# Kernel tuning notes

Hardware: AMD Instinct MI355X
Metric: run time of the kernel (lower is better)

## Reference

```python
import jax, jax.numpy as jnp
import numpy as np

H = 1024   # hidden_size
NH = 16    # num heads
HD = H // NH


def setup_inputs() -> dict:
    key = jax.random.key(0)
    ks = jax.random.split(key, 6)
    B, S = 4, 2048
    hidden_states = jax.random.normal(ks[0], (B, S, H), dtype=jnp.float32)
    attention_mask = jnp.zeros((B, S), dtype=jnp.float32)  # additive mask
    scale = 1.0 / np.sqrt(H)
    Wq = jax.random.normal(ks[1], (H, H), dtype=jnp.float32) * scale
    Wk = jax.random.normal(ks[2], (H, H), dtype=jnp.float32) * scale
    Wv = jax.random.normal(ks[3], (H, H), dtype=jnp.float32) * scale
    Wo = jax.random.normal(ks[4], (H, H), dtype=jnp.float32) * scale
    return {"hidden_states": hidden_states, "attention_mask": attention_mask,
            "Wq": Wq, "Wk": Wk, "Wv": Wv, "Wo": Wo}


def reference(hidden_states, attention_mask, Wq, Wk, Wv, Wo):
    B, S, _ = hidden_states.shape
    scaling = HD ** -0.5
    # nn.Linear: y = x @ W.T ; split heads -> [B, NH, S, HD]
    def heads(x, W):
        return (x @ W.T).reshape(B, S, NH, HD).transpose(0, 2, 1, 3)
    q = heads(hidden_states, Wq)
    k = heads(hidden_states, Wk)
    v = heads(hidden_states, Wv)
    scores = jnp.einsum('bhqd,bhkd->bhqk', q, k) * scaling
    scores = scores + attention_mask[:, None, None, :]
    weights = jax.nn.softmax(scores, axis=-1)
    attn = jnp.einsum('bhqk,bhkd->bhqd', weights, v)
    attn = attn.transpose(0, 2, 1, 3).reshape(B, S, H)
    return attn @ Wo.T
```

## Files before the change

kernel.cpp:

```cpp
#include <hip/hip_runtime.h>
#include <hip/hip_bf16.h>

#define B_ 4
#define S_ 2048
#define H_ 1024
#define NH_ 16
#define HD_ 64
#define QSCALE 0.1803368801111204f

typedef __bf16 bf16_t;
typedef bf16_t bf16x8 __attribute__((ext_vector_type(8)));
typedef bf16_t bf16x4 __attribute__((ext_vector_type(4)));
typedef bf16_t bf16x2t __attribute__((ext_vector_type(2)));
typedef float f32x4 __attribute__((ext_vector_type(4)));
typedef unsigned u32x2 __attribute__((ext_vector_type(2)));
typedef unsigned u32x4 __attribute__((ext_vector_type(4)));

__device__ __forceinline__ f32x4 mfma16(bf16x8 a, bf16x8 b, f32x4 c) {
  return __builtin_amdgcn_mfma_f32_16x16x32_bf16(a, b, c, 0, 0, 0);
}

__device__ __forceinline__ float fast_exp2(float x) {
#if __has_builtin(__builtin_amdgcn_exp2f)
  return __builtin_amdgcn_exp2f(x);
#else
  float r;
  asm volatile("v_exp_f32 %0, %1" : "=v"(r) : "v"(x));
  return r;
#endif
}

__device__ __forceinline__ void gll16(const bf16_t* g, bf16_t* l) {
  __builtin_amdgcn_global_load_lds(
      (const __attribute__((address_space(1))) void*)g,
      (__attribute__((address_space(3))) void*)l, 16, 0, 0);
}

__device__ __forceinline__ bf16x8 frag64(const bf16_t* lds, int row,
                                         int kchunk) {
  return *(const bf16x8*)((const char*)lds + row * 128 +
                          ((kchunk ^ (row & 7)) << 4));
}

__device__ __forceinline__ void stage128(const bf16_t* gbase, int gstride,
                                         bf16_t* lds, int w, int lane) {
#pragma unroll
  for (int j = 0; j < 4; ++j) {
    int seg = w * 4 + j;
    int row = seg * 8 + (lane >> 3);
    int chunk = (lane & 7) ^ (row & 7);
    gll16(gbase + (size_t)row * gstride + chunk * 8, lds + seg * 512);
  }
}

__global__ __launch_bounds__(256) void cvt_all(
    const float* __restrict__ X, const float* __restrict__ Wq,
    const float* __restrict__ Wk, const float* __restrict__ Wv,
    const float* __restrict__ Wo, const float* __restrict__ mask,
    bf16_t* __restrict__ Xb, bf16_t* __restrict__ Wqb,
    bf16_t* __restrict__ Wkb, bf16_t* __restrict__ Wvb,
    bf16_t* __restrict__ Wob, float* __restrict__ maskl) {
  size_t i = ((size_t)blockIdx.x * 256 + threadIdx.x) * 4;
  const float* src;
  bf16_t* dst;
  size_t off;
  float scale = 1.0f;
  if (i < 8388608) {
    src = X; dst = Xb; off = i;
  } else {
    size_t j = i - 8388608;
    if (j >= 4194304) {
      size_t mo = j - 4194304;
      float4 mv = *(const float4*)(mask + mo);
      const float LOG2E = 1.4426950408889634f;
      float4 ml = {mv.x * LOG2E, mv.y * LOG2E, mv.z * LOG2E, mv.w * LOG2E};
      *(float4*)(maskl + mo) = ml;
      return;
    }
    int w = (int)(j >> 20);
    off = j & 1048575;
    switch (w) {
      case 0: src = Wq; dst = Wqb; scale = QSCALE; break;
      case 1: src = Wk; dst = Wkb; break;
      case 2: src = Wv; dst = Wvb; break;
      default: src = Wo; dst = Wob; break;
    }
  }
  float4 v = *(const float4*)(src + off);
  bf16x4 o = {(bf16_t)(v.x * scale), (bf16_t)(v.y * scale),
              (bf16_t)(v.z * scale), (bf16_t)(v.w * scale)};
  *(bf16x4*)(dst + off) = o;
}

__device__ __forceinline__ void gemm_core(const bf16_t* __restrict__ A,
                                          const bf16_t* __restrict__ Bw,
                                          int Mb, int Nb, bf16_t* As,
                                          bf16_t* Bs, f32x4 (*acc)[4], int w,
                                          int lane, int quad, int l15, int wm,
                                          int wn) {
  for (int kb = 0; kb < 16; ++kb) {
    stage128(A + (size_t)Mb * 1024 + kb * 64, 1024, As, w, lane);
    stage128(Bw + (size_t)Nb * 1024 + kb * 64, 1024, Bs, w, lane);
    __syncthreads();
#pragma unroll
    for (int kt = 0; kt < 2; ++kt) {
      bf16x8 af[4], bfr[4];
#pragma unroll
      for (int i = 0; i < 4; ++i) {
        af[i] = frag64(As, wm * 64 + i * 16 + l15, kt * 4 + quad);
        bfr[i] = frag64(Bs, wn * 64 + i * 16 + l15, kt * 4 + quad);
      }
      __builtin_amdgcn_s_setprio(1);
#pragma unroll
      for (int mt = 0; mt < 4; ++mt)
#pragma unroll
        for (int nt = 0; nt < 4; ++nt)
          acc[mt][nt] = mfma16(af[mt], bfr[nt], acc[mt][nt]);
      __builtin_amdgcn_s_setprio(0);
    }
    __syncthreads();
  }
}

__global__ __launch_bounds__(256) void gemm_qkv(
    const bf16_t* __restrict__ Xb, const bf16_t* __restrict__ Wqb,
    const bf16_t* __restrict__ Wkb, const bf16_t* __restrict__ Wvb,
    bf16_t* __restrict__ q_ws, bf16_t* __restrict__ k_ws,
    bf16_t* __restrict__ vt_ws) {
  __shared__ __align__(16) bf16_t As[8192];
  __shared__ __align__(16) bf16_t Bs[8192];
  int w = threadIdx.x >> 6, lane = threadIdx.x & 63;
  int quad = lane >> 4, l15 = lane & 15;
  int wm = w >> 1, wn = w & 1;
  int z = blockIdx.z;
  const bf16_t* A = (z == 2) ? Wvb : Xb;
  const bf16_t* Bw = (z == 0) ? Wqb : ((z == 1) ? Wkb : Xb);
  int Mb = (z == 2) ? blockIdx.y * 128 : blockIdx.x * 128;
  int Nb = (z == 2) ? blockIdx.x * 128 : blockIdx.y * 128;
  f32x4 acc[4][4] = {};
  gemm_core(A, Bw, Mb, Nb, As, Bs, acc, w, lane, quad, l15, wm, wn);
  if (z != 2) {
    bf16_t* O = (z == 0) ? q_ws : k_ws;
#pragma unroll
    for (int mt = 0; mt < 4; ++mt) {
      int m0t = Mb + wm * 64 + mt * 16;
#pragma unroll
      for (int nt = 0; nt < 4; ++nt) {
        int n0t = Nb + wn * 64 + nt * 16;
        int h = n0t >> 6, d = (n0t & 63) + l15;
#pragma unroll
        for (int r = 0; r < 4; ++r) {
          int tok = m0t + quad * 4 + r;
          int b = tok >> 11, s = tok & 2047;
          O[(((size_t)b * NH_ + h) * S_ + s) * HD_ + d] = (bf16_t)acc[mt][nt][r];
        }
      }
    }
  } else {
#pragma unroll
    for (int mt = 0; mt < 4; ++mt) {
      int m0t = Mb + wm * 64 + mt * 16;
#pragma unroll
      for (int nt = 0; nt < 4; ++nt) {
        int n0t = Nb + wn * 64 + nt * 16;
#pragma unroll
        for (int r = 0; r < 4; ++r) {
          int dg = m0t + quad * 4 + r;
          int hh = dg >> 6, d = dg & 63;
          int tok = n0t + l15;
          int b = tok >> 11, s = tok & 2047;
          vt_ws[((size_t)(b * NH_ + hh) * HD_ + d) * S_ + s] =
              (bf16_t)acc[mt][nt][r];
        }
      }
    }
  }
}

__global__ __launch_bounds__(256) void gemm_out(
    const bf16_t* __restrict__ A, const bf16_t* __restrict__ Bw,
    float* __restrict__ out) {
  __shared__ __align__(16) bf16_t As[8192];
  __shared__ __align__(16) bf16_t Bs[8192];
  int w = threadIdx.x >> 6, lane = threadIdx.x & 63;
  int quad = lane >> 4, l15 = lane & 15;
  int wm = w >> 1, wn = w & 1;
  int Mb = blockIdx.x * 128, Nb = blockIdx.y * 128;
  f32x4 acc[4][4] = {};
  gemm_core(A, Bw, Mb, Nb, As, Bs, acc, w, lane, quad, l15, wm, wn);
#pragma unroll
  for (int mt = 0; mt < 4; ++mt) {
    int m0t = Mb + wm * 64 + mt * 16;
#pragma unroll
    for (int nt = 0; nt < 4; ++nt) {
      int n0t = Nb + wn * 64 + nt * 16;
#pragma unroll
      for (int r = 0; r < 4; ++r)
        out[(size_t)(m0t + quad * 4 + r) * 1024 + n0t + l15] = acc[mt][nt][r];
    }
  }
}

__global__ __launch_bounds__(256, 3) void attn_fused(
    const bf16_t* __restrict__ Q, const bf16_t* __restrict__ K,
    const bf16_t* __restrict__ Vt, const float* __restrict__ maskl,
    bf16_t* __restrict__ Oa) {
  __shared__ __align__(16) bf16_t Ks[2][4096];
  __shared__ __align__(16) bf16_t Vs[2][4096];
  int w = threadIdx.x >> 6, lane = threadIdx.x & 63;
  int quad = lane >> 4, l15 = lane & 15;
  int bh = blockIdx.y;
  int b = bh >> 4, h = bh & 15;
  int q0 = blockIdx.x * 128 + w * 32;
  const bf16_t* Qh = Q + (size_t)bh * (S_ * HD_);
  const bf16_t* Kh = K + (size_t)bh * (S_ * HD_);
  const bf16_t* Vh = Vt + (size_t)bh * (HD_ * S_);
  const float* mb = maskl + b * S_;
  const bf16_t one_b = (bf16_t)1.0f;
  bf16x8 ones = {one_b, one_b, one_b, one_b, one_b, one_b, one_b, one_b};

  int srow[2], schunk[2], soff[2];
#pragma unroll
  for (int j = 0; j < 2; ++j) {
    int seg = w * 2 + j;
    srow[j] = seg * 8 + (lane >> 3);
    schunk[j] = (lane & 7) ^ (srow[j] & 7);
    soff[j] = seg * 512 + lane * 8;
  }

  bf16x8 qf[2][2];
#pragma unroll
  for (int nt = 0; nt < 2; ++nt)
#pragma unroll
    for (int kt = 0; kt < 2; ++kt)
      qf[nt][kt] = *(const bf16x8*)(Qh + (size_t)(q0 + nt * 16 + l15) * HD_ +
                                    kt * 32 + quad * 8);

  f32x4 oc[4][2] = {};
  f32x4 lc[2] = {};

  bf16x8 kreg[2], vreg[2];
#pragma unroll
  for (int j = 0; j < 2; ++j) {
    kreg[j] = *(const bf16x8*)(Kh + (size_t)srow[j] * HD_ + schunk[j] * 8);
    vreg[j] = *(const bf16x8*)(Vh + (size_t)srow[j] * S_ + schunk[j] * 8);
  }
#pragma unroll
  for (int j = 0; j < 2; ++j) {
    *(bf16x8*)(&Ks[0][0] + soff[j]) = kreg[j];
    *(bf16x8*)(&Vs[0][0] + soff[j]) = vreg[j];
  }
#pragma unroll
  for (int j = 0; j < 2; ++j) {
    kreg[j] = *(const bf16x8*)(Kh + (size_t)(64 * HD_) +
                               (size_t)srow[j] * HD_ + schunk[j] * 8);
    vreg[j] = *(const bf16x8*)(Vh + 64 + (size_t)srow[j] * S_ + schunk[j] * 8);
  }
  f32x4 mreg[4];
#pragma unroll
  for (int mt = 0; mt < 4; ++mt)
    mreg[mt] = *(const f32x4*)(mb + mt * 16 + quad * 4);
  __syncthreads();

  for (int c = 0; c < 32; ++c) {
    int cur = c & 1;
    if (c + 1 < 32) {
#pragma unroll
      for (int j = 0; j < 2; ++j) {
        *(bf16x8*)(&Ks[cur ^ 1][0] + soff[j]) = kreg[j];
        *(bf16x8*)(&Vs[cur ^ 1][0] + soff[j]) = vreg[j];
      }
    }
    if (c + 2 < 32) {
      const bf16_t* Kc = Kh + (size_t)(c + 2) * 64 * HD_;
      const bf16_t* Vc = Vh + (size_t)(c + 2) * 64;
#pragma unroll
      for (int j = 0; j < 2; ++j) {
        kreg[j] = *(const bf16x8*)(Kc + (size_t)srow[j] * HD_ + schunk[j] * 8);
        vreg[j] = *(const bf16x8*)(Vc + (size_t)srow[j] * S_ + schunk[j] * 8);
      }
    }
    f32x4 mcur[4];
#pragma unroll
    for (int mt = 0; mt < 4; ++mt) mcur[mt] = mreg[mt];
    if (c + 1 < 32) {
#pragma unroll
      for (int mt = 0; mt < 4; ++mt)
        mreg[mt] = *(const f32x4*)(mb + (c + 1) * 64 + mt * 16 + quad * 4);
    }
    f32x4 sc[4][2] = {};
#pragma unroll
    for (int kt = 0; kt < 2; ++kt) {
      bf16x8 kf[4];
#pragma unroll
      for (int mt = 0; mt < 4; ++mt)
        kf[mt] = frag64(Ks[cur], mt * 16 + l15, kt * 4 + quad);
      __builtin_amdgcn_s_setprio(1);
#pragma unroll
      for (int mt = 0; mt < 4; ++mt)
#pragma unroll
        for (int nt = 0; nt < 2; ++nt)
          sc[mt][nt] = mfma16(kf[mt], qf[nt][kt], sc[mt][nt]);
      __builtin_amdgcn_s_setprio(0);
    }
#pragma unroll
    for (int kt = 0; kt < 2; ++kt) {
      unsigned pk[2][2][2];
#pragma unroll
      for (int mi = 0; mi < 2; ++mi) {
        int mt = kt * 2 + mi;
#pragma unroll
        for (int nt = 0; nt < 2; ++nt) {
          f32x4 e = sc[mt][nt] + mcur[mt];
          f32x4 p;
#pragma unroll
          for (int r = 0; r < 4; ++r) p[r] = fast_exp2(e[r]);
          bf16x2t h0 = {(bf16_t)p[0], (bf16_t)p[1]};
          bf16x2t h1 = {(bf16_t)p[2], (bf16_t)p[3]};
          pk[mi][nt][0] = __builtin_bit_cast(unsigned, h0);
          pk[mi][nt][1] = __builtin_bit_cast(unsigned, h1);
        }
      }
      bf16x8 pf[2];
#pragma unroll
      for (int nt = 0; nt < 2; ++nt) {
        u32x2 a0 = __builtin_amdgcn_permlane32_swap(pk[0][nt][0],
                                                    pk[1][nt][0],
                                                    false, false);
        u32x2 b0 = __builtin_amdgcn_permlane16_swap(a0.x, a0.y, false, false);
        u32x2 a1 = __builtin_amdgcn_permlane32_swap(pk[0][nt][1],
                                                    pk[1][nt][1],
                                                    false, false);
        u32x2 b1 = __builtin_amdgcn_permlane16_swap(a1.x, a1.y, false, false);
        u32x4 pu = {b0.x, b1.x, b0.y, b1.y};
        pf[nt] = __builtin_bit_cast(bf16x8, pu);
      }
      __builtin_amdgcn_s_setprio(1);
      lc[0] = mfma16(ones, pf[0], lc[0]);
      lc[1] = mfma16(ones, pf[1], lc[1]);
#pragma unroll
      for (int dt = 0; dt < 4; ++dt) {
        bf16x8 vf = frag64(Vs[cur], dt * 16 + l15, kt * 4 + quad);
#pragma unroll
        for (int nt = 0; nt < 2; ++nt)
          oc[dt][nt] = mfma16(vf, pf[nt], oc[dt][nt]);
      }
      __builtin_amdgcn_s_setprio(0);
    }
    __syncthreads();
  }
  float inv[2] = {1.0f / lc[0][0], 1.0f / lc[1][0]};
#pragma unroll
  for (int dt = 0; dt < 4; ++dt)
#pragma unroll
    for (int nt = 0; nt < 2; ++nt) {
      bf16x4 o4;
#pragma unroll
      for (int r = 0; r < 4; ++r) o4[r] = (bf16_t)(oc[dt][nt][r] * inv[nt]);
      size_t tok = (size_t)b * S_ + q0 + nt * 16 + l15;
      *(bf16x4*)(Oa + tok * H_ + h * HD_ + dt * 16 + quad * 4) = o4;
    }
}

extern "C" void kernel_launch(void* const* d_in, const int* in_sizes, int n_in,
                              void* d_out, int out_size, void* d_ws,
                              size_t ws_size, hipStream_t stream) {
  const float* hs   = (const float*)d_in[0];
  const float* mask = (const float*)d_in[1];
  const float* Wq   = (const float*)d_in[2];
  const float* Wk   = (const float*)d_in[3];
  const float* Wv   = (const float*)d_in[4];
  const float* Wo   = (const float*)d_in[5];
  float* out = (float*)d_out;

  char* p = (char*)d_ws;
  bf16_t* Xb  = (bf16_t*)p; p += (size_t)8192 * 1024 * 2;
  bf16_t* Wqb = (bf16_t*)p; p += (size_t)1024 * 1024 * 2;
  bf16_t* Wkb = (bf16_t*)p; p += (size_t)1024 * 1024 * 2;
  bf16_t* Wvb = (bf16_t*)p; p += (size_t)1024 * 1024 * 2;
  bf16_t* Wob = (bf16_t*)p; p += (size_t)1024 * 1024 * 2;
  bf16_t* q_ws  = (bf16_t*)p; p += (size_t)8192 * 1024 * 2;
  bf16_t* k_ws  = (bf16_t*)p; p += (size_t)8192 * 1024 * 2;
  bf16_t* vt_ws = (bf16_t*)p; p += (size_t)8192 * 1024 * 2;
  float* maskl = (float*)p; p += (size_t)B_ * S_ * 4;
  bf16_t* attn_b = Xb;

  cvt_all<<<12296, 256, 0, stream>>>(hs, Wq, Wk, Wv, Wo, mask, Xb, Wqb, Wkb,
                                     Wvb, Wob, maskl);
  gemm_qkv<<<dim3(64, 8, 3), 256, 0, stream>>>(Xb, Wqb, Wkb, Wvb, q_ws, k_ws,
                                               vt_ws);
  attn_fused<<<dim3(16, 64), 256, 0, stream>>>(q_ws, k_ws, vt_ws, maskl,
                                               attn_b);
  gemm_out<<<dim3(64, 8), 256, 0, stream>>>(attn_b, Wob, out);
}
```

Baseline: 304.0 us.

## Stage K/V tiles via direct global-to-LDS loads and drop setprio hints

Replaces the register-staged double buffering of K and V tiles (global load into VGPRs, then an LDS store one iteration later) with direct global_load_lds transfers straight into the alternate LDS buffer, prefetching one chunk ahead instead of two. The aim is to free VGPRs and remove the LDS write instructions and their latency from the main loop. It also removes the s_setprio wrappers around the MFMA blocks and switches exp2 to the OCML native exp2. The prefetch distance shrinks and correctness now depends on the async LDS loads being complete before the barrier.

```diff
diff --git a/kernel.cpp b/kernel.cpp
--- a/kernel.cpp
+++ b/kernel.cpp
@@ -20,14 +20,9 @@
   return __builtin_amdgcn_mfma_f32_16x16x32_bf16(a, b, c, 0, 0, 0);
 }
 
+extern "C" __device__ float __ocml_native_exp2_f32(float);
 __device__ __forceinline__ float fast_exp2(float x) {
-#if __has_builtin(__builtin_amdgcn_exp2f)
-  return __builtin_amdgcn_exp2f(x);
-#else
-  float r;
-  asm volatile("v_exp_f32 %0, %1" : "=v"(r) : "v"(x));
-  return r;
-#endif
+  return __ocml_native_exp2_f32(x);
 }
 
 __device__ __forceinline__ void gll16(const bf16_t* g, bf16_t* l) {
@@ -219,13 +214,13 @@
   const bf16_t one_b = (bf16_t)1.0f;
   bf16x8 ones = {one_b, one_b, one_b, one_b, one_b, one_b, one_b, one_b};
 
-  int srow[2], schunk[2], soff[2];
+  int srow[2], schunk[2], lseg[2];
 #pragma unroll
   for (int j = 0; j < 2; ++j) {
     int seg = w * 2 + j;
     srow[j] = seg * 8 + (lane >> 3);
     schunk[j] = (lane & 7) ^ (srow[j] & 7);
-    soff[j] = seg * 512 + lane * 8;
+    lseg[j] = seg * 512;
   }
 
   bf16x8 qf[2][2];
@@ -239,22 +234,10 @@
   f32x4 oc[4][2] = {};
   f32x4 lc[2] = {};
 
-  bf16x8 kreg[2], vreg[2];
 #pragma unroll
   for (int j = 0; j < 2; ++j) {
-    kreg[j] = *(const bf16x8*)(Kh + (size_t)srow[j] * HD_ + schunk[j] * 8);
-    vreg[j] = *(const bf16x8*)(Vh + (size_t)srow[j] * S_ + schunk[j] * 8);
-  }
-#pragma unroll
-  for (int j = 0; j < 2; ++j) {
-    *(bf16x8*)(&Ks[0][0] + soff[j]) = kreg[j];
-    *(bf16x8*)(&Vs[0][0] + soff[j]) = vreg[j];
-  }
-#pragma unroll
-  for (int j = 0; j < 2; ++j) {
-    kreg[j] = *(const bf16x8*)(Kh + (size_t)(64 * HD_) +
-                               (size_t)srow[j] * HD_ + schunk[j] * 8);
-    vreg[j] = *(const bf16x8*)(Vh + 64 + (size_t)srow[j] * S_ + schunk[j] * 8);
+    gll16(Kh + (size_t)srow[j] * HD_ + schunk[j] * 8, &Ks[0][0] + lseg[j]);
+    gll16(Vh + (size_t)srow[j] * S_ + schunk[j] * 8, &Vs[0][0] + lseg[j]);
   }
   f32x4 mreg[4];
 #pragma unroll
@@ -265,19 +248,14 @@
   for (int c = 0; c < 32; ++c) {
     int cur = c & 1;
     if (c + 1 < 32) {
+      const bf16_t* Kc = Kh + (size_t)(c + 1) * 64 * HD_;
+      const bf16_t* Vc = Vh + (size_t)(c + 1) * 64;
 #pragma unroll
       for (int j = 0; j < 2; ++j) {
-        *(bf16x8*)(&Ks[cur ^ 1][0] + soff[j]) = kreg[j];
-        *(bf16x8*)(&Vs[cur ^ 1][0] + soff[j]) = vreg[j];
-      }
-    }
-    if (c + 2 < 32) {
-      const bf16_t* Kc = Kh + (size_t)(c + 2) * 64 * HD_;
-      const bf16_t* Vc = Vh + (size_t)(c + 2) * 64;
-#pragma unroll
-      for (int j = 0; j < 2; ++j) {
-        kreg[j] = *(const bf16x8*)(Kc + (size_t)srow[j] * HD_ + schunk[j] * 8);
-        vreg[j] = *(const bf16x8*)(Vc + (size_t)srow[j] * S_ + schunk[j] * 8);
+        gll16(Kc + (size_t)srow[j] * HD_ + schunk[j] * 8,
+              &Ks[cur ^ 1][0] + lseg[j]);
+        gll16(Vc + (size_t)srow[j] * S_ + schunk[j] * 8,
+              &Vs[cur ^ 1][0] + lseg[j]);
       }
     }
     f32x4 mcur[4];
@@ -295,13 +273,11 @@
 #pragma unroll
       for (int mt = 0; mt < 4; ++mt)
         kf[mt] = frag64(Ks[cur], mt * 16 + l15, kt * 4 + quad);
-      __builtin_amdgcn_s_setprio(1);
 #pragma unroll
       for (int mt = 0; mt < 4; ++mt)
 #pragma unroll
         for (int nt = 0; nt < 2; ++nt)
           sc[mt][nt] = mfma16(kf[mt], qf[nt][kt], sc[mt][nt]);
-      __builtin_amdgcn_s_setprio(0);
     }
 #pragma unroll
     for (int kt = 0; kt < 2; ++kt) {
@@ -335,7 +311,6 @@
         u32x4 pu = {b0.x, b1.x, b0.y, b1.y};
         pf[nt] = __builtin_bit_cast(bf16x8, pu);
       }
-      __builtin_amdgcn_s_setprio(1);
       lc[0] = mfma16(ones, pf[0], lc[0]);
       lc[1] = mfma16(ones, pf[1], lc[1]);
 #pragma unroll
@@ -345,7 +320,6 @@
         for (int nt = 0; nt < 2; ++nt)
           oc[dt][nt] = mfma16(vf, pf[nt], oc[dt][nt]);
       }
-      __builtin_amdgcn_s_setprio(0);
     }
     __syncthreads();
   }
```

Result: faster. 270.8 us (-10.9%).
